# Optimization experiments

Measured on AMD Instinct MI355X. Metric: run time of the kernel, lower is better.

## Reference

```python
import jax, jax.numpy as jnp
import numpy as np

V, K, D, RH, RC = 50257, 1024, 1024, 384, 32
B, T = 2, 2048


def setup_inputs() -> dict:
    key = jax.random.key(0)
    k_tok, k_bh, k_bc, k_uh, k_uc = jax.random.split(key, 5)
    return {
        "tokens": jax.random.randint(k_tok, (B, T), 0, V, dtype=jnp.int32),
        "old_to_new": jnp.arange(V, dtype=jnp.int32),  # default hot_ids=arange(K) -> identity perm
        "B_hot": jax.random.normal(k_bh, (RH, D), dtype=jnp.float32) / np.sqrt(RH),
        "B_cold": jax.random.normal(k_bc, (RC, D), dtype=jnp.float32) / np.sqrt(RC),
        "U_hot": jax.random.normal(k_uh, (K, RH), dtype=jnp.float32) / np.sqrt(RH),
        "U_cold": jax.random.normal(k_uc, (V - K, RC), dtype=jnp.float32) / np.sqrt(RC),
        "log_alpha": jnp.zeros((), dtype=jnp.float32),
        "out_bias": jnp.zeros((V,), dtype=jnp.float32),
    }


def reference(tokens, old_to_new, B_hot, B_cold, U_hot, U_cold, log_alpha, out_bias):
    k_hot = U_hot.shape[0]
    # ---- encode: hot/cold masked gather -> low-rank matmul -> select ----
    tok_new = old_to_new[tokens]                       # [B, T]
    is_hot = tok_new < k_hot
    hot_idx = jnp.where(is_hot, tok_new, 0)
    cold_idx = jnp.where(is_hot, 0, tok_new - k_hot)
    emb_hot = U_hot[hot_idx] @ B_hot                   # [B, T, d]
    emb_cold = U_cold[cold_idx] @ B_cold               # [B, T, d]
    latent = jnp.where(is_hot[..., None], emb_hot, emb_cold)
    # ---- decode: tied low-rank logits, block-wise, reorder + scale + bias ----
    alpha = jnp.exp(log_alpha)
    hot_logits = (latent @ B_hot.T) @ U_hot.T          # [B, T, K]
    cold_logits = (latent @ B_cold.T) @ U_cold.T       # [B, T, V-K]
    logits_new = jnp.concatenate([hot_logits, cold_logits], axis=-1)
    logits = jnp.take(logits_new, old_to_new, axis=-1)  # index_select over V
    return logits * alpha + out_bias
```

## Files before the change

kernel.cpp:

```cpp
#include <hip/hip_runtime.h>
#include <hip/hip_bf16.h>

#define VOUT 50257
#define KHOT 1024
#define DIM  1024
#define RHOT 384
#define RCOLD 32
#define RF   416

typedef __attribute__((ext_vector_type(8))) short short8;
typedef __attribute__((ext_vector_type(4))) float f32x4;

__global__ void k_convert(const float* __restrict__ Bh, const float* __restrict__ Bc,
                          const float* __restrict__ Uh, const float* __restrict__ Uc,
                          __hip_bfloat16* __restrict__ Bmat,
                          __hip_bfloat16* __restrict__ UhB,
                          __hip_bfloat16* __restrict__ UcB) {
  const int nBh = RHOT * DIM;
  const int nBm = RF * DIM;
  const int nUh = KHOT * RHOT;
  const int nUc = (VOUT - KHOT) * RCOLD;
  const int total = nBm + nUh + nUc;
  for (int i = blockIdx.x * blockDim.x + threadIdx.x; i < total;
       i += gridDim.x * blockDim.x) {
    if (i < nBm) {
      float v = (i < nBh) ? Bh[i] : Bc[i - nBh];
      Bmat[i] = __float2bfloat16(v);
    } else if (i < nBm + nUh) {
      UhB[i - nBm] = __float2bfloat16(Uh[i - nBm]);
    } else {
      int j = i - nBm - nUh;
      UcB[j] = __float2bfloat16(Uc[j]);
    }
  }
}

__global__ __launch_bounds__(256) void k_gram(const __hip_bfloat16* __restrict__ Bmat,
                                              float* __restrict__ G) {
  const int wave = threadIdx.x >> 6;
  const int lane = threadIdx.x & 63;
  const int idx = blockIdx.x * 4 + wave;
  if (idx >= 26 * 26) return;
  const int ti = idx / 26, tj = idx % 26;
  const int i0 = ti * 16, j0 = tj * 16;
  const int col16 = lane & 15;
  const int g4 = lane >> 4;

  f32x4 acc = (f32x4){0.f, 0.f, 0.f, 0.f};
  const __hip_bfloat16* arow = Bmat + (size_t)(i0 + col16) * DIM;
  const __hip_bfloat16* brow = Bmat + (size_t)(j0 + col16) * DIM;
#pragma unroll 4
  for (int ks = 0; ks < DIM / 32; ++ks) {
    short8 a = *reinterpret_cast<const short8*>(arow + ks * 32 + g4 * 8);
    short8 b = *reinterpret_cast<const short8*>(brow + ks * 32 + g4 * 8);
    acc = __builtin_amdgcn_mfma_f32_16x16x32_bf16(a, b, acc, 0, 0, 0);
  }
#pragma unroll
  for (int r = 0; r < 4; ++r)
    G[(size_t)(i0 + g4 * 4 + r) * RF + j0 + col16] = acc[r];
}

__global__ void k_encode(const int* __restrict__ tokens, const int* __restrict__ o2n,
                         const float* __restrict__ Uh, const float* __restrict__ Uc,
                         const float* __restrict__ G, __hip_bfloat16* __restrict__ F) {
  const int n = blockIdx.x;
  __shared__ float u[RHOT];
  const int tok = tokens[n];
  const int tn = o2n[tok];
  const bool hot = tn < KHOT;
  const int R = hot ? RHOT : RCOLD;
  const float* urow = hot ? (Uh + (size_t)tn * RHOT) : (Uc + (size_t)(tn - KHOT) * RCOLD);
  for (int r = threadIdx.x; r < R; r += blockDim.x) u[r] = urow[r];
  __syncthreads();
  const int gbase = hot ? 0 : RHOT;
  for (int c = threadIdx.x; c < RF; c += blockDim.x) {
    float acc = 0.f;
    for (int r = 0; r < R; ++r) acc += u[r] * G[(size_t)(gbase + r) * RF + c];
    F[(size_t)n * RF + c] = __float2bfloat16(acc);
  }
}

#define CPB 256
#define RPB 64

__global__ __launch_bounds__(256) void k_out(const int* __restrict__ o2n,
                                             const __hip_bfloat16* __restrict__ F,
                                             const __hip_bfloat16* __restrict__ Uh,
                                             const __hip_bfloat16* __restrict__ Uc,
                                             const float* __restrict__ log_alpha,
                                             const float* __restrict__ bias,
                                             float* __restrict__ out) {
  __shared__ __hip_bfloat16 Fc[RPB][40];
  __shared__ float Epi[16][260];
  const int tid = threadIdx.x;
  const int wave = tid >> 6;
  const int lane = tid & 63;
  const int col16 = lane & 15;
  const int g4 = lane >> 4;
  const int n0 = blockIdx.y * RPB;
  const int cbase = blockIdx.x * CPB;
  const float alpha = expf(log_alpha[0]);
  const short8 zero8 = (short8){0, 0, 0, 0, 0, 0, 0, 0};

  {
    const int row = tid >> 2, chunk = tid & 3;
    short8 v = *reinterpret_cast<const short8*>(F + (size_t)(n0 + row) * RF + RHOT + chunk * 8);
    *reinterpret_cast<short8*>(&Fc[row][chunk * 8]) = v;
  }
  __syncthreads();

  int src[4];
  float bv[4];
  bool hotcs[4];
#pragma unroll
  for (int cs = 0; cs < 4; ++cs) {
    const int v = cbase + wave * 64 + cs * 16 + col16;
    const int vc = (v < VOUT) ? v : (VOUT - 1);
    src[cs] = o2n[vc];
    bv[cs] = bias[vc];
    hotcs[cs] = __any(src[cs] < KHOT);
  }

  f32x4 acc[4][4];
#pragma unroll
  for (int cs = 0; cs < 4; ++cs)
#pragma unroll
    for (int t = 0; t < 4; ++t) acc[cs][t] = (f32x4){0.f, 0.f, 0.f, 0.f};

  {
    short8 afc[4];
#pragma unroll
    for (int t = 0; t < 4; ++t)
      afc[t] = *reinterpret_cast<const short8*>(&Fc[t * 16 + col16][g4 * 8]);
#pragma unroll
    for (int cs = 0; cs < 4; ++cs) {
      if (__any(src[cs] >= KHOT)) {
        short8 bfrag = zero8;
        if (src[cs] >= KHOT)
          bfrag = *reinterpret_cast<const short8*>(Uc + (size_t)(src[cs] - KHOT) * RCOLD + g4 * 8);
#pragma unroll
        for (int t = 0; t < 4; ++t)
          acc[cs][t] = __builtin_amdgcn_mfma_f32_16x16x32_bf16(afc[t], bfrag, acc[cs][t], 0, 0, 0);
      }
    }
  }
  if (hotcs[0] | hotcs[1] | hotcs[2] | hotcs[3]) {
    for (int ks = 0; ks < RHOT / 32; ++ks) {
      short8 afh[4];
#pragma unroll
      for (int t = 0; t < 4; ++t)
        afh[t] = *reinterpret_cast<const short8*>(
            F + (size_t)(n0 + t * 16 + col16) * RF + ks * 32 + g4 * 8);
#pragma unroll
      for (int cs = 0; cs < 4; ++cs) {
        if (hotcs[cs]) {
          short8 bfrag = zero8;
          if (src[cs] < KHOT)
            bfrag = *reinterpret_cast<const short8*>(Uh + (size_t)src[cs] * RHOT + ks * 32 + g4 * 8);
#pragma unroll
          for (int t = 0; t < 4; ++t)
            acc[cs][t] = __builtin_amdgcn_mfma_f32_16x16x32_bf16(afh[t], bfrag, acc[cs][t], 0, 0, 0);
        }
      }
    }
  }

  for (int t = 0; t < 4; ++t) {
    __syncthreads();
#pragma unroll
    for (int cs = 0; cs < 4; ++cs) {
#pragma unroll
      for (int r = 0; r < 4; ++r)
        Epi[g4 * 4 + r][wave * 64 + cs * 16 + col16] = acc[cs][t][r] * alpha + bv[cs];
    }
    __syncthreads();
#pragma unroll
    for (int rr = 0; rr < 4; ++rr) {
      const int row = wave * 4 + rr;
      f32x4 vals = *reinterpret_cast<const f32x4*>(&Epi[row][lane * 4]);
      const size_t gr = (size_t)(n0 + t * 16 + row) * VOUT;
      const int c0 = cbase + lane * 4;
      if (c0 + 3 < VOUT) {
        *reinterpret_cast<f32x4*>(out + gr + c0) = vals;
      } else {
#pragma unroll
        for (int j = 0; j < 4; ++j)
          if (c0 + j < VOUT) out[gr + c0 + j] = vals[j];
      }
    }
  }
}

extern "C" void kernel_launch(void* const* d_in, const int* in_sizes, int n_in,
                              void* d_out, int out_size, void* d_ws, size_t ws_size,
                              hipStream_t stream) {
  const int* tokens    = (const int*)d_in[0];
  const int* o2n       = (const int*)d_in[1];
  const float* B_hot   = (const float*)d_in[2];
  const float* B_cold  = (const float*)d_in[3];
  const float* U_hot   = (const float*)d_in[4];
  const float* U_cold  = (const float*)d_in[5];
  const float* log_a   = (const float*)d_in[6];
  const float* bias    = (const float*)d_in[7];
  float* out = (float*)d_out;

  const int N = in_sizes[0];

  char* ws = (char*)d_ws;
  __hip_bfloat16* Bmat = (__hip_bfloat16*)(ws + 0);
  __hip_bfloat16* UhB  = (__hip_bfloat16*)(ws + (1u << 20));
  __hip_bfloat16* UcB  = (__hip_bfloat16*)(ws + (2u << 20));
  float*          G    = (float*)(ws + (6u << 20));
  __hip_bfloat16* F    = (__hip_bfloat16*)(ws + (7u << 20));

  k_convert<<<2048, 256, 0, stream>>>(B_hot, B_cold, U_hot, U_cold, Bmat, UhB, UcB);
  k_gram<<<169, 256, 0, stream>>>(Bmat, G);
  k_encode<<<N, 256, 0, stream>>>(tokens, o2n, U_hot, U_cold, G, F);

  dim3 grid((VOUT + CPB - 1) / CPB, N / RPB);
  k_out<<<grid, 256, 0, stream>>>(o2n, F, UhB, UcB, log_a, bias, out);
}
```

Before: 322.5 us.

## Widen output tiles to 1024 columns and swizzle block order across XCDs

Each block of the logits kernel now covers 1024 vocabulary columns instead of 256. It loops over the four 16-row slabs with 16 accumulator fragments, so each F fragment load is reused across more columns. Block indices are also remapped so consecutive tiles land on the same XCD, which is meant to improve L2 locality. The costs are higher register pressure from 16 per-lane source, bias and accumulator arrays, four times fewer blocks, and extra barriers in the epilogue.

```diff
diff --git a/kernel.cpp b/kernel.cpp
--- a/kernel.cpp
+++ b/kernel.cpp
@@ -80,7 +80,7 @@
   }
 }
 
-#define CPB 256
+#define CPB 1024
 #define RPB 64
 
 __global__ __launch_bounds__(256) void k_out(const int* __restrict__ o2n,
@@ -97,8 +97,16 @@
   const int lane = tid & 63;
   const int col16 = lane & 15;
   const int g4 = lane >> 4;
-  const int n0 = blockIdx.y * RPB;
-  const int cbase = blockIdx.x * CPB;
+
+  const int nx = gridDim.x;
+  const int L = blockIdx.y * nx + blockIdx.x;
+  const int ntot = nx * gridDim.y;
+  const int T = (L >> 3) + (L & 7) * (ntot >> 3);
+  const int tx = T % nx;
+  const int ty = T / nx;
+  const int n0 = ty * RPB;
+  const int cb = tx * CPB;
+
   const float alpha = expf(log_alpha[0]);
   const short8 zero8 = (short8){0, 0, 0, 0, 0, 0, 0, 0};
 
@@ -107,86 +115,81 @@
     short8 v = *reinterpret_cast<const short8*>(F + (size_t)(n0 + row) * RF + RHOT + chunk * 8);
     *reinterpret_cast<short8*>(&Fc[row][chunk * 8]) = v;
   }
+
+  int srcs[16];
+  float bvk[16];
+  unsigned hotmask = 0, coldmask = 0;
+#pragma unroll
+  for (int i = 0; i < 16; ++i) {
+    const int s = i >> 2, k = i & 3;
+    const int v = cb + s * 256 + wave * 64 + k * 16 + col16;
+    const int vc = (v < VOUT) ? v : (VOUT - 1);
+    srcs[i] = o2n[vc];
+    bvk[i] = bias[vc];
+    if (__any(srcs[i] < KHOT)) hotmask |= (1u << i);
+    if (__any(srcs[i] >= KHOT)) coldmask |= (1u << i);
+  }
   __syncthreads();
 
-  int src[4];
-  float bv[4];
-  bool hotcs[4];
-#pragma unroll
-  for (int cs = 0; cs < 4; ++cs) {
-    const int v = cbase + wave * 64 + cs * 16 + col16;
-    const int vc = (v < VOUT) ? v : (VOUT - 1);
-    src[cs] = o2n[vc];
-    bv[cs] = bias[vc];
-    hotcs[cs] = __any(src[cs] < KHOT);
-  }
-
-  f32x4 acc[4][4];
-#pragma unroll
-  for (int cs = 0; cs < 4; ++cs)
-#pragma unroll
-    for (int t = 0; t < 4; ++t) acc[cs][t] = (f32x4){0.f, 0.f, 0.f, 0.f};
-
-  {
-    short8 afc[4];
-#pragma unroll
-    for (int t = 0; t < 4; ++t)
-      afc[t] = *reinterpret_cast<const short8*>(&Fc[t * 16 + col16][g4 * 8]);
-#pragma unroll
-    for (int cs = 0; cs < 4; ++cs) {
-      if (__any(src[cs] >= KHOT)) {
-        short8 bfrag = zero8;
-        if (src[cs] >= KHOT)
-          bfrag = *reinterpret_cast<const short8*>(Uc + (size_t)(src[cs] - KHOT) * RCOLD + g4 * 8);
-#pragma unroll
-        for (int t = 0; t < 4; ++t)
-          acc[cs][t] = __builtin_amdgcn_mfma_f32_16x16x32_bf16(afc[t], bfrag, acc[cs][t], 0, 0, 0);
-      }
-    }
-  }
-  if (hotcs[0] | hotcs[1] | hotcs[2] | hotcs[3]) {
-    for (int ks = 0; ks < RHOT / 32; ++ks) {
-      short8 afh[4];
-#pragma unroll
-      for (int t = 0; t < 4; ++t)
-        afh[t] = *reinterpret_cast<const short8*>(
+  for (int t = 0; t < 4; ++t) {
+    f32x4 acc[16];
+#pragma unroll
+    for (int i = 0; i < 16; ++i) acc[i] = (f32x4){0.f, 0.f, 0.f, 0.f};
+
+    {
+      const short8 afc = *reinterpret_cast<const short8*>(&Fc[t * 16 + col16][g4 * 8]);
+#pragma unroll
+      for (int i = 0; i < 16; ++i) {
+        if (coldmask & (1u << i)) {
+          short8 bfrag = zero8;
+          if (srcs[i] >= KHOT)
+            bfrag = *reinterpret_cast<const short8*>(
+                Uc + (size_t)(srcs[i] - KHOT) * RCOLD + g4 * 8);
+          acc[i] = __builtin_amdgcn_mfma_f32_16x16x32_bf16(afc, bfrag, acc[i], 0, 0, 0);
+        }
+      }
+    }
+    if (hotmask) {
+      for (int ks = 0; ks < RHOT / 32; ++ks) {
+        const short8 afh = *reinterpret_cast<const short8*>(
             F + (size_t)(n0 + t * 16 + col16) * RF + ks * 32 + g4 * 8);
 #pragma unroll
-      for (int cs = 0; cs < 4; ++cs) {
-        if (hotcs[cs]) {
-          short8 bfrag = zero8;
-          if (src[cs] < KHOT)
-            bfrag = *reinterpret_cast<const short8*>(Uh + (size_t)src[cs] * RHOT + ks * 32 + g4 * 8);
-#pragma unroll
-          for (int t = 0; t < 4; ++t)
-            acc[cs][t] = __builtin_amdgcn_mfma_f32_16x16x32_bf16(afh[t], bfrag, acc[cs][t], 0, 0, 0);
+        for (int i = 0; i < 16; ++i) {
+          if (hotmask & (1u << i)) {
+            short8 bfrag = zero8;
+            if (srcs[i] < KHOT)
+              bfrag = *reinterpret_cast<const short8*>(
+                  Uh + (size_t)srcs[i] * RHOT + ks * 32 + g4 * 8);
+            acc[i] = __builtin_amdgcn_mfma_f32_16x16x32_bf16(afh, bfrag, acc[i], 0, 0, 0);
+          }
         }
       }
     }
-  }
-
-  for (int t = 0; t < 4; ++t) {
-    __syncthreads();
-#pragma unroll
-    for (int cs = 0; cs < 4; ++cs) {
-#pragma unroll
-      for (int r = 0; r < 4; ++r)
-        Epi[g4 * 4 + r][wave * 64 + cs * 16 + col16] = acc[cs][t][r] * alpha + bv[cs];
-    }
-    __syncthreads();
-#pragma unroll
-    for (int rr = 0; rr < 4; ++rr) {
-      const int row = wave * 4 + rr;
-      f32x4 vals = *reinterpret_cast<const f32x4*>(&Epi[row][lane * 4]);
-      const size_t gr = (size_t)(n0 + t * 16 + row) * VOUT;
-      const int c0 = cbase + lane * 4;
-      if (c0 + 3 < VOUT) {
-        *reinterpret_cast<f32x4*>(out + gr + c0) = vals;
-      } else {
-#pragma unroll
-        for (int j = 0; j < 4; ++j)
-          if (c0 + j < VOUT) out[gr + c0 + j] = vals[j];
-      }
+
+    for (int s = 0; s < 4; ++s) {
+#pragma unroll
+      for (int k = 0; k < 4; ++k) {
+        const int i = s * 4 + k;
+#pragma unroll
+        for (int r = 0; r < 4; ++r)
+          Epi[g4 * 4 + r][wave * 64 + k * 16 + col16] = acc[i][r] * alpha + bvk[i];
+      }
+      __syncthreads();
+#pragma unroll
+      for (int rr = 0; rr < 4; ++rr) {
+        const int row = wave * 4 + rr;
+        f32x4 vals = *reinterpret_cast<const f32x4*>(&Epi[row][lane * 4]);
+        const size_t gr = (size_t)(n0 + t * 16 + row) * VOUT;
+        const int c0 = cb + s * 256 + lane * 4;
+        if (c0 + 3 < VOUT) {
+          *reinterpret_cast<f32x4*>(out + gr + c0) = vals;
+        } else {
+#pragma unroll
+          for (int j = 0; j < 4; ++j)
+            if (c0 + j < VOUT) out[gr + c0 + j] = vals[j];
+        }
+      }
+      __syncthreads();
     }
   }
 }
```

After: 484.0 us. 50.1% more time.
